# Kernel optimization log

Hardware: AMD Instinct MI355X
Metric: run time of the kernel (lower is better)

The kernel has to match this reference:

```python
import jax, jax.numpy as jnp
import numpy as np

B, K, H, W = 8, 1024, 24, 24
C = H * W            # in_channels = 576
NH = 6               # hardcoded num_heads
HD = C // NH         # 96


def setup_inputs() -> dict:
    key = jax.random.key(0)
    ks = jax.random.split(key, 8)
    s = 1.0 / np.sqrt(C)
    return {
        "input1": jax.random.normal(ks[0], (B, K, H, W), jnp.float32),
        "input2": jax.random.normal(ks[1], (B, K, H, W), jnp.float32),
        "Wq": jax.random.uniform(ks[2], (C, C), jnp.float32, -s, s),
        "bq": jax.random.uniform(ks[3], (C,), jnp.float32, -s, s),
        "Wk": jax.random.uniform(ks[4], (C, C), jnp.float32, -s, s),
        "bk": jax.random.uniform(ks[5], (C,), jnp.float32, -s, s),
        "Wv": jax.random.uniform(ks[6], (C, C), jnp.float32, -s, s),
        "bv": jax.random.uniform(ks[7], (C,), jnp.float32, -s, s),
    }


def reference(input1, input2, Wq, bq, Wk, bk, Wv, bv):
    b, k, h, w = input1.shape
    c = h * w
    x1 = input1.reshape(b, k, c)
    x2 = input2.reshape(b, k, c)
    # torch nn.Linear: y = x @ W^T + b
    q = x1 @ Wq.T + bq                      # [b, k, c]
    kk = x2 @ Wk.T + bk
    v = x2 @ Wv.T + bv
    # torch .view scrambles: [b, k, c] -> [b, NH, c//NH, k] (row-major reshape)
    q = q.reshape(b, NH, c // NH, k)
    kk = kk.reshape(b, NH, c // NH, k)
    v = v.reshape(b, NH, c // NH, k)
    # scores = q^T k over head-dim; NOTE: no 1/sqrt(d) scaling in original
    scores = jnp.einsum('bhdq,bhdk->bhqk', q, kk)   # [b, NH, k, k]
    weights = jax.nn.softmax(scores, axis=-1)
    # context = value @ weights^T -> [b, NH, hd, k]
    ctx = jnp.einsum('bhdk,bhqk->bhdq', v, weights)
    return ctx.reshape(b, k, h, w)
```

## Files before the change

kernel.cpp:

```cpp
#include <hip/hip_runtime.h>
#include <cmath>

#define BATCH 8
#define KDIM  1024
#define CH    576
#define NHEAD 6
#define HDIM  96

typedef _Float16 f16;
typedef f16 f16x4 __attribute__((ext_vector_type(4)));
typedef f16 f16x8 __attribute__((ext_vector_type(8)));
typedef float f32x16 __attribute__((ext_vector_type(16)));

__device__ inline f32x16 zero16() {
    f32x16 z;
#pragma unroll
    for (int r = 0; r < 16; ++r) z[r] = 0.f;
    return z;
}

__global__ __launch_bounds__(256) void proj_kernel(
    const float* __restrict__ x1, const float* __restrict__ x2,
    const float* __restrict__ Wq, const float* __restrict__ Wk,
    const float* __restrict__ Wv,
    const float* __restrict__ bq, const float* __restrict__ bk,
    const float* __restrict__ bv,
    f16* __restrict__ qf, f16* __restrict__ kf, f16* __restrict__ vf)
{
    const int z = blockIdx.z;
    const float* A    = (z == 0) ? x1 : x2;
    const float* W    = (z == 0) ? Wq : (z == 1) ? Wk : Wv;
    const float* bias = (z == 0) ? bq : (z == 1) ? bk : bv;
    f16* dst          = (z == 0) ? qf : (z == 1) ? kf : vf;

    __shared__ f16 As[128 * 72];
    __shared__ f16 Ws[192 * 72];

    const int tid = threadIdx.x;
    const int lane = tid & 63, w = tid >> 6;
    const int l31 = lane & 31, half = lane >> 5;
    const int nBase = blockIdx.x * 192;
    const int mBase = blockIdx.y * 128;

    f32x16 acc[6] = {zero16(), zero16(), zero16(), zero16(), zero16(), zero16()};

    for (int k0 = 0; k0 < CH; k0 += 64) {
        __syncthreads();
#pragma unroll
        for (int r = 0; r < 4; ++r) {
            int idx = r * 256 + tid;
            int row = idx >> 3, ch = idx & 7;
            const float* src = &A[(size_t)(mBase + row) * CH + k0 + ch * 8];
            float4 u0 = *(const float4*)src;
            float4 u1 = *(const float4*)(src + 4);
            f16x8 hv;
            hv[0] = (f16)u0.x; hv[1] = (f16)u0.y; hv[2] = (f16)u0.z; hv[3] = (f16)u0.w;
            hv[4] = (f16)u1.x; hv[5] = (f16)u1.y; hv[6] = (f16)u1.z; hv[7] = (f16)u1.w;
            *(f16x8*)&As[row * 72 + ch * 8] = hv;
        }
#pragma unroll
        for (int r = 0; r < 6; ++r) {
            int idx = r * 256 + tid;
            int row = idx >> 3, ch = idx & 7;
            const float* src = &W[(size_t)(nBase + row) * CH + k0 + ch * 8];
            float4 u0 = *(const float4*)src;
            float4 u1 = *(const float4*)(src + 4);
            f16x8 hv;
            hv[0] = (f16)u0.x; hv[1] = (f16)u0.y; hv[2] = (f16)u0.z; hv[3] = (f16)u0.w;
            hv[4] = (f16)u1.x; hv[5] = (f16)u1.y; hv[6] = (f16)u1.z; hv[7] = (f16)u1.w;
            *(f16x8*)&Ws[row * 72 + ch * 8] = hv;
        }
        __syncthreads();
#pragma unroll
        for (int ks = 0; ks < 4; ++ks) {
            f16x8 a = *(const f16x8*)&As[(32 * w + l31) * 72 + 16 * ks + 8 * half];
#pragma unroll
            for (int nt = 0; nt < 6; ++nt) {
                f16x8 bfr = *(const f16x8*)&Ws[(32 * nt + l31) * 72 + 16 * ks + 8 * half];
                acc[nt] = __builtin_amdgcn_mfma_f32_32x32x16_f16(a, bfr, acc[nt], 0, 0, 0);
            }
        }
    }

#pragma unroll
    for (int nt = 0; nt < 6; ++nt) {
        int n = nBase + 32 * nt + l31;
        float bsv = bias[n];
#pragma unroll
        for (int r = 0; r < 16; ++r) {
            int m = mBase + 32 * w + (r & 3) + 8 * (r >> 2) + 4 * half;
            dst[(size_t)m * CH + n] = (f16)(acc[nt][r] + bsv);
        }
    }
}

__global__ __launch_bounds__(256) void transpose_qk(
    const f16* __restrict__ qf, const f16* __restrict__ kf,
    f16* __restrict__ QT, f16* __restrict__ KT)
{
    const int tt = blockIdx.x;
    const int bh = blockIdx.y;
    const f16* src = blockIdx.z ? kf : qf;
    f16* dst = blockIdx.z ? KT : QT;

    __shared__ f16 Ts[96 * 72];

    const int tid = threadIdx.x;
    const int rowbase = (bh / NHEAD) * CH + (bh % NHEAD) * HDIM;

#pragma unroll
    for (int r = 0; r < 3; ++r) {
        int idx = r * 256 + tid;
        int d = idx >> 3, g = idx & 7;
        *(f16x8*)&Ts[d * 72 + g * 8] =
            *(const f16x8*)&src[(size_t)(rowbase + d) * KDIM + tt * 64 + g * 8];
    }
    __syncthreads();
#pragma unroll
    for (int r = 0; r < 3; ++r) {
        int idx = r * 256 + tid;
        int t = idx & 63, dg = idx >> 6;
        f16x8 v;
#pragma unroll
        for (int u = 0; u < 8; ++u) v[u] = Ts[(dg * 8 + u) * 72 + t];
        *(f16x8*)&dst[((size_t)bh * KDIM + tt * 64 + t) * HDIM + dg * 8] = v;
    }
}

__global__ __launch_bounds__(256, 3) void attn_kernel(
    const f16* __restrict__ qT, const f16* __restrict__ kT,
    const f16* __restrict__ vf, float* __restrict__ out)
{
    __shared__ __align__(16) char smem[49664];
    f16* Qs = (f16*)smem;
    f16* Ks = (f16*)(smem + 13312);
    f16* Ps = (f16*)(smem + 26624);
    f16* Vs = (f16*)(smem + 35840);

    const int qt = blockIdx.x;
    const int h  = blockIdx.y;
    const int b  = blockIdx.z;
    const int bh = b * NHEAD + h;

    const int tid = threadIdx.x;
    const int lane = tid & 63, w = tid >> 6;
    const int ih = w & 1, jg = w >> 1;
    const int l31 = lane & 31, half = lane >> 5;
    const int iw = 32 * ih;

    const f16* Qbase = qT + ((size_t)bh * KDIM + qt * 64) * HDIM;
    const f16* Kbase = kT + (size_t)bh * KDIM * HDIM;
    const f16* Vbase = vf + ((size_t)b * CH + (size_t)h * HDIM) * KDIM;

#pragma unroll
    for (int r = 0; r < 3; ++r) {
        int idx = r * 256 + tid;
        int t = idx / 12, g = idx % 12;
        *(f16x8*)&Qs[t * 104 + g * 8] = *(const f16x8*)&Qbase[t * 96 + g * 8];
    }
    __syncthreads();

    f16x8 qfr[6];
#pragma unroll
    for (int ks = 0; ks < 6; ++ks)
        qfr[ks] = *(const f16x8*)&Qs[(iw + l31) * 104 + 16 * ks + 8 * half];

    float m_run = -INFINITY, l_run = 0.f;
    f32x16 Oacc[3] = {zero16(), zero16(), zero16()};

    for (int jt = 0; jt < KDIM; jt += 64) {
        __syncthreads();
#pragma unroll
        for (int r = 0; r < 3; ++r) {
            int idx = r * 256 + tid;
            int t = idx / 12, g = idx % 12;
            *(f16x8*)&Ks[t * 104 + g * 8] =
                *(const f16x8*)&Kbase[(size_t)(jt + t) * HDIM + g * 8];
        }
#pragma unroll
        for (int r = 0; r < 3; ++r) {
            int idx = r * 256 + tid;
            int d = idx >> 3, g = idx & 7;
            *(f16x8*)&Vs[d * 72 + g * 8] =
                *(const f16x8*)&Vbase[(size_t)d * KDIM + jt + g * 8];
        }
        __syncthreads();

        f32x16 s0 = zero16();
#pragma unroll
        for (int ks = 0; ks < 6; ++ks) {
            f16x8 ak = *(const f16x8*)&Ks[(32 * jg + l31) * 104 + 16 * ks + 8 * half];
            s0 = __builtin_amdgcn_mfma_f32_32x32x16_f16(ak, qfr[ks], s0, 0, 0, 0);
        }

        float mx = -INFINITY;
#pragma unroll
        for (int r = 0; r < 16; ++r) mx = fmaxf(mx, s0[r]);
        mx = fmaxf(mx, __shfl_xor(mx, 32));
        float mnew = fmaxf(m_run, mx);
        float alpha = __expf(m_run - mnew);
        m_run = mnew;
        float sum = 0.f;
        f16x4 pq[4];
#pragma unroll
        for (int r = 0; r < 16; ++r) {
            float e = __expf(s0[r] - mnew);
            sum += e;
            pq[r >> 2][r & 3] = (f16)e;
        }
        sum += __shfl_xor(sum, 32);
        l_run = alpha * l_run + sum;

#pragma unroll
        for (int q = 0; q < 4; ++q)
            *(f16x4*)&Ps[(iw + l31) * 72 + 32 * jg + 8 * q + 4 * half] = pq[q];

        if (__any(alpha != 1.0f)) {
#pragma unroll
            for (int t = 0; t < 3; ++t)
#pragma unroll
                for (int r = 0; r < 16; ++r) Oacc[t][r] *= alpha;
        }

#pragma unroll
        for (int kc = 0; kc < 2; ++kc) {
            int jo = 32 * jg + 16 * kc + 8 * half;
            f16x8 bp = *(const f16x8*)&Ps[(iw + l31) * 72 + jo];
#pragma unroll
            for (int t = 0; t < 3; ++t) {
                f16x8 av = *(const f16x8*)&Vs[(32 * t + l31) * 72 + jo];
                Oacc[t] = __builtin_amdgcn_mfma_f32_32x32x16_f16(av, bp, Oacc[t], 0, 0, 0);
            }
        }
    }

    __syncthreads();
    float* Oscr = (float*)smem;
    float* mScr = (float*)(smem + 26624);
    float* lScr = (float*)(smem + 26880);
    if (jg == 1) {
        if (half == 0) { mScr[iw + l31] = m_run; lScr[iw + l31] = l_run; }
        float* od = Oscr + ih * 3168;
#pragma unroll
        for (int t = 0; t < 3; ++t)
#pragma unroll
            for (int r = 0; r < 16; ++r) {
                int d = 32 * t + (r & 3) + 8 * (r >> 2) + 4 * half;
                od[d * 33 + l31] = Oacc[t][r];
            }
    }
    __syncthreads();
    if (jg == 0) {
        float m1 = mScr[iw + l31], l1 = lScr[iw + l31];
        float mstar = fmaxf(m_run, m1);
        float a0 = __expf(m_run - mstar), a1 = __expf(m1 - mstar);
        float linv = 1.0f / (l_run * a0 + l1 * a1);
        const float* od = Oscr + ih * 3168;
        float* obase = out + ((size_t)b * CH + (size_t)h * HDIM) * KDIM
                           + qt * 64 + iw + l31;
#pragma unroll
        for (int t = 0; t < 3; ++t)
#pragma unroll
            for (int r = 0; r < 16; ++r) {
                int d = 32 * t + (r & 3) + 8 * (r >> 2) + 4 * half;
                obase[(size_t)d * KDIM] =
                    (Oacc[t][r] * a0 + od[d * 33 + l31] * a1) * linv;
            }
    }
}

extern "C" void kernel_launch(void* const* d_in, const int* in_sizes, int n_in,
                              void* d_out, int out_size, void* d_ws, size_t ws_size,
                              hipStream_t stream)
{
    const float* x1 = (const float*)d_in[0];
    const float* x2 = (const float*)d_in[1];
    const float* Wq = (const float*)d_in[2];
    const float* bq = (const float*)d_in[3];
    const float* Wk = (const float*)d_in[4];
    const float* bk = (const float*)d_in[5];
    const float* Wv = (const float*)d_in[6];
    const float* bv = (const float*)d_in[7];
    float* out = (float*)d_out;

    const size_t P = (size_t)BATCH * KDIM * CH;
    f16* qf = (f16*)d_ws;
    f16* kf = qf + P;
    f16* vf = kf + P;
    f16* QT = vf + P;
    f16* KT = QT + P;

    dim3 pgrid(CH / 192, (BATCH * KDIM) / 128, 3);
    proj_kernel<<<pgrid, 256, 0, stream>>>(x1, x2, Wq, Wk, Wv,
                                           bq, bk, bv, qf, kf, vf);

    dim3 tgrid(KDIM / 64, BATCH * NHEAD, 2);
    transpose_qk<<<tgrid, 256, 0, stream>>>(qf, kf, QT, KT);

    dim3 agrid(KDIM / 64, NHEAD, BATCH);
    attn_kernel<<<agrid, 256, 0, stream>>>(QT, KT, vf, out);
}
```

Before: 182.4 us.

## Prefetch K/V tiles into registers, pass P via lane shuffles, shrink projection tile

```diff
diff --git a/kernel.cpp b/kernel.cpp
--- a/kernel.cpp
+++ b/kernel.cpp
@@ -11,6 +11,7 @@
 typedef f16 f16x4 __attribute__((ext_vector_type(4)));
 typedef f16 f16x8 __attribute__((ext_vector_type(8)));
 typedef float f32x16 __attribute__((ext_vector_type(16)));
+typedef unsigned int u32;
 
 __device__ inline f32x16 zero16() {
     f32x16 z;
@@ -34,15 +35,15 @@
     f16* dst          = (z == 0) ? qf : (z == 1) ? kf : vf;
 
     __shared__ f16 As[128 * 72];
-    __shared__ f16 Ws[192 * 72];
+    __shared__ f16 Ws[96 * 72];
 
     const int tid = threadIdx.x;
     const int lane = tid & 63, w = tid >> 6;
     const int l31 = lane & 31, half = lane >> 5;
-    const int nBase = blockIdx.x * 192;
+    const int nBase = blockIdx.x * 96;
     const int mBase = blockIdx.y * 128;
 
-    f32x16 acc[6] = {zero16(), zero16(), zero16(), zero16(), zero16(), zero16()};
+    f32x16 acc[3] = {zero16(), zero16(), zero16()};
 
     for (int k0 = 0; k0 < CH; k0 += 64) {
         __syncthreads();
@@ -59,7 +60,7 @@
             *(f16x8*)&As[row * 72 + ch * 8] = hv;
         }
 #pragma unroll
-        for (int r = 0; r < 6; ++r) {
+        for (int r = 0; r < 3; ++r) {
             int idx = r * 256 + tid;
             int row = idx >> 3, ch = idx & 7;
             const float* src = &W[(size_t)(nBase + row) * CH + k0 + ch * 8];
@@ -75,7 +76,7 @@
         for (int ks = 0; ks < 4; ++ks) {
             f16x8 a = *(const f16x8*)&As[(32 * w + l31) * 72 + 16 * ks + 8 * half];
 #pragma unroll
-            for (int nt = 0; nt < 6; ++nt) {
+            for (int nt = 0; nt < 3; ++nt) {
                 f16x8 bfr = *(const f16x8*)&Ws[(32 * nt + l31) * 72 + 16 * ks + 8 * half];
                 acc[nt] = __builtin_amdgcn_mfma_f32_32x32x16_f16(a, bfr, acc[nt], 0, 0, 0);
             }
@@ -83,7 +84,7 @@
     }
 
 #pragma unroll
-    for (int nt = 0; nt < 6; ++nt) {
+    for (int nt = 0; nt < 3; ++nt) {
         int n = nBase + 32 * nt + l31;
         float bsv = bias[n];
 #pragma unroll
@@ -131,11 +132,10 @@
     const f16* __restrict__ qT, const f16* __restrict__ kT,
     const f16* __restrict__ vf, float* __restrict__ out)
 {
-    __shared__ __align__(16) char smem[49664];
-    f16* Qs = (f16*)smem;
-    f16* Ks = (f16*)(smem + 13312);
-    f16* Ps = (f16*)(smem + 26624);
-    f16* Vs = (f16*)(smem + 35840);
+    __shared__ __align__(16) char smem[27136];
+    f16* Ks = (f16*)smem;
+    f16* Vs = (f16*)(smem + 13312);
+    f16* Qs = Ks;
 
     const int qt = blockIdx.x;
     const int h  = blockIdx.y;
@@ -152,19 +152,31 @@
     const f16* Kbase = kT + (size_t)bh * KDIM * HDIM;
     const f16* Vbase = vf + ((size_t)b * CH + (size_t)h * HDIM) * KDIM;
 
+    int kt[3], kg[3], vd[3], vg[3];
 #pragma unroll
     for (int r = 0; r < 3; ++r) {
         int idx = r * 256 + tid;
-        int t = idx / 12, g = idx % 12;
-        *(f16x8*)&Qs[t * 104 + g * 8] = *(const f16x8*)&Qbase[t * 96 + g * 8];
-    }
+        kt[r] = idx / 12; kg[r] = idx % 12;
+        vd[r] = idx >> 3; vg[r] = idx & 7;
+    }
+
+#pragma unroll
+    for (int r = 0; r < 3; ++r)
+        *(f16x8*)&Qs[kt[r] * 104 + kg[r] * 8] =
+            *(const f16x8*)&Qbase[kt[r] * 96 + kg[r] * 8];
     __syncthreads();
-
     f16x8 qfr[6];
 #pragma unroll
     for (int ks = 0; ks < 6; ++ks)
         qfr[ks] = *(const f16x8*)&Qs[(iw + l31) * 104 + 16 * ks + 8 * half];
 
+    f16x8 kreg[3], vreg[3];
+#pragma unroll
+    for (int r = 0; r < 3; ++r) {
+        kreg[r] = *(const f16x8*)&Kbase[(size_t)kt[r] * HDIM + kg[r] * 8];
+        vreg[r] = *(const f16x8*)&Vbase[(size_t)vd[r] * KDIM + vg[r] * 8];
+    }
+
     float m_run = -INFINITY, l_run = 0.f;
     f32x16 Oacc[3] = {zero16(), zero16(), zero16()};
 
@@ -172,19 +184,17 @@
         __syncthreads();
 #pragma unroll
         for (int r = 0; r < 3; ++r) {
-            int idx = r * 256 + tid;
-            int t = idx / 12, g = idx % 12;
-            *(f16x8*)&Ks[t * 104 + g * 8] =
-                *(const f16x8*)&Kbase[(size_t)(jt + t) * HDIM + g * 8];
-        }
-#pragma unroll
-        for (int r = 0; r < 3; ++r) {
-            int idx = r * 256 + tid;
-            int d = idx >> 3, g = idx & 7;
-            *(f16x8*)&Vs[d * 72 + g * 8] =
-                *(const f16x8*)&Vbase[(size_t)d * KDIM + jt + g * 8];
+            *(f16x8*)&Ks[kt[r] * 104 + kg[r] * 8] = kreg[r];
+            *(f16x8*)&Vs[vd[r] * 72 + vg[r] * 8]  = vreg[r];
         }
         __syncthreads();
+        if (jt + 64 < KDIM) {
+#pragma unroll
+            for (int r = 0; r < 3; ++r) {
+                kreg[r] = *(const f16x8*)&Kbase[(size_t)(jt + 64 + kt[r]) * HDIM + kg[r] * 8];
+                vreg[r] = *(const f16x8*)&Vbase[(size_t)vd[r] * KDIM + jt + 64 + vg[r] * 8];
+            }
+        }
 
         f32x16 s0 = zero16();
 #pragma unroll
@@ -211,10 +221,6 @@
         sum += __shfl_xor(sum, 32);
         l_run = alpha * l_run + sum;
 
-#pragma unroll
-        for (int q = 0; q < 4; ++q)
-            *(f16x4*)&Ps[(iw + l31) * 72 + 32 * jg + 8 * q + 4 * half] = pq[q];
-
         if (__any(alpha != 1.0f)) {
 #pragma unroll
             for (int t = 0; t < 3; ++t)
@@ -224,8 +230,20 @@
 
 #pragma unroll
         for (int kc = 0; kc < 2; ++kc) {
+            union { f16x4 h; u32 u[2]; } snd, rcv, keep;
+            keep.h = half ? pq[2 * kc + 1] : pq[2 * kc];
+            snd.h  = half ? pq[2 * kc]     : pq[2 * kc + 1];
+            rcv.u[0] = __shfl_xor((int)snd.u[0], 32);
+            rcv.u[1] = __shfl_xor((int)snd.u[1], 32);
+            f16x8 bp;
+            if (half == 0) {
+#pragma unroll
+                for (int v = 0; v < 4; ++v) { bp[v] = keep.h[v]; bp[4 + v] = rcv.h[v]; }
+            } else {
+#pragma unroll
+                for (int v = 0; v < 4; ++v) { bp[v] = rcv.h[v]; bp[4 + v] = keep.h[v]; }
+            }
             int jo = 32 * jg + 16 * kc + 8 * half;
-            f16x8 bp = *(const f16x8*)&Ps[(iw + l31) * 72 + jo];
 #pragma unroll
             for (int t = 0; t < 3; ++t) {
                 f16x8 av = *(const f16x8*)&Vs[(32 * t + l31) * 72 + jo];
@@ -236,8 +254,8 @@
 
     __syncthreads();
     float* Oscr = (float*)smem;
-    float* mScr = (float*)(smem + 26624);
-    float* lScr = (float*)(smem + 26880);
+    float* mScr = (float*)(smem + 25344);
+    float* lScr = (float*)(smem + 25600);
     if (jg == 1) {
         if (half == 0) { mScr[iw + l31] = m_run; lScr[iw + l31] = l_run; }
         float* od = Oscr + ih * 3168;
@@ -290,7 +308,7 @@
     f16* QT = vf + P;
     f16* KT = QT + P;
 
-    dim3 pgrid(CH / 192, (BATCH * KDIM) / 128, 3);
+    dim3 pgrid(CH / 96, (BATCH * KDIM) / 128, 3);
     proj_kernel<<<pgrid, 256, 0, stream>>>(x1, x2, Wq, Wk, Wv,
                                            bq, bk, bv, qf, kf, vf);
 
```

Result: slower. 190.4 us (+4.4%).
